# Performance work log

Hardware: AMD Instinct MI355X
Metric: run time of the kernel (lower is better)

Reference implementation:

```python
import jax, jax.numpy as jnp
import numpy as np

B, S, D, H = 8, 2048, 1024, 16
HD = D // H  # head_dim = 64


def setup_inputs() -> dict:
    key = jax.random.key(0)
    ks = jax.random.split(key, 10)
    s = 0.02
    return {
        "x": jax.random.normal(ks[0], (B, S, D), jnp.float32),
        "mask": jnp.zeros((B, 1, S), jnp.float32),
        "Wq": jax.random.normal(ks[1], (D, D), jnp.float32) * s,
        "bq": jnp.zeros((D,), jnp.float32),
        "Wk": jax.random.normal(ks[2], (D, D), jnp.float32) * s,
        "bk": jnp.zeros((D,), jnp.float32),
        "Wv": jax.random.normal(ks[3], (D, D), jnp.float32) * s,
        "bv": jnp.zeros((D,), jnp.float32),
        "wa": jax.random.normal(ks[4], (HD, 1), jnp.float32) * s,
        "ba": jnp.zeros((1,), jnp.float32),
        "wb": jax.random.normal(ks[5], (HD, 1), jnp.float32) * s,
        "bb": jnp.zeros((1,), jnp.float32),
        "Wu": jax.random.normal(ks[6], (HD, HD), jnp.float32) * s,
        "bu": jnp.zeros((HD,), jnp.float32),
        "Wo": jax.random.normal(ks[7], (D, D), jnp.float32) * s,
        "bo": jnp.zeros((D,), jnp.float32),
        "gamma": jnp.ones((D,), jnp.float32),
        "beta_ln": jnp.zeros((D,), jnp.float32),
    }


def _split_heads(t):
    # [B,S,D] -> [B,H,S,HD]
    return t.reshape(B, S, H, HD).transpose(0, 2, 1, 3)


def reference(x, mask, Wq, bq, Wk, bk, Wv, bv, wa, ba, wb, bb, Wu, bu, Wo, bo, gamma, beta_ln):
    scale = 1.0 / jnp.sqrt(jnp.float32(HD))
    q = _split_heads(x @ Wq + bq)  # [B,H,S,HD]
    k = _split_heads(x @ Wk + bk)
    v = _split_heads(x @ Wv + bv)

    # additive attention over queries -> global query vector per head
    alphascore = (jnp.squeeze(q @ wa, -1) + ba[0]) * scale + mask  # [B,H,S]
    alphaw = jax.nn.softmax(alphascore, axis=-1)
    q_av = jnp.einsum('bhs,bhsd->bhd', alphaw, q)

    p = k * q_av[:, :, None, :]  # gated keys [B,H,S,HD]
    betascore = (jnp.squeeze(p @ wb, -1) + bb[0]) * scale + mask
    betaw = jax.nn.softmax(betascore, axis=-1)
    p_av = jnp.einsum('bhs,bhsd->bhd', betaw, p)

    u = v * p_av[:, :, None, :]  # gated values
    r = u @ Wu + bu  # [B,H,S,HD]
    newr = (r + q).transpose(0, 2, 1, 3).reshape(B, S, D)
    attn_out = newr @ Wo + bo

    h = x + attn_out
    mu = jnp.mean(h, axis=-1, keepdims=True)
    var = jnp.mean(jnp.square(h - mu), axis=-1, keepdims=True)
    return (h - mu) * jax.lax.rsqrt(var + 1e-6) * gamma + beta_ln
```

## Files before the change

kernel.cpp:

```cpp
#include <hip/hip_runtime.h>
#include <cstdint>

#define BB 8
#define SS 2048
#define DD 1024
#define HH 16
#define HDIM 64
#define MTOT (BB*SS)
#define NQKV 3072

typedef __attribute__((ext_vector_type(8))) __bf16 bf16x8;
typedef __attribute__((ext_vector_type(4))) float f32x4;

#define AS1(p) ((const __attribute__((address_space(1))) void*)(p))
#define AS3(p) ((__attribute__((address_space(3))) void*)(p))

__device__ __forceinline__ float bf2f(uint16_t u){
  return __uint_as_float(((uint32_t)u) << 16);
}
__device__ __forceinline__ uint16_t f2bf(float f){
  uint32_t u = __float_as_uint(f);
  return (uint16_t)((u + 0x7fffu + ((u >> 16) & 1u)) >> 16);
}

__global__ __launch_bounds__(256)
void k_prep(const float* __restrict__ x,
            const float* __restrict__ Wq, const float* __restrict__ Wk,
            const float* __restrict__ Wv, const float* __restrict__ Wo,
            const float* __restrict__ bq, const float* __restrict__ bk,
            const float* __restrict__ bv,
            uint16_t* __restrict__ xb, uint16_t* __restrict__ Wt,
            uint16_t* __restrict__ WoT, float* __restrict__ bqkv)
{
  __shared__ float t[32][33];
  const int blk = blockIdx.x, tid = threadIdx.x;
  if (blk < 2048){
    const int n4 = MTOT*DD/4;
    for (int i = blk*256 + tid; i < n4; i += 2048*256){
      float4 v = reinterpret_cast<const float4*>(x)[i];
      ushort4 o;
      o.x = f2bf(v.x); o.y = f2bf(v.y); o.z = f2bf(v.z); o.w = f2bf(v.w);
      reinterpret_cast<ushort4*>(xb)[i] = o;
    }
  } else if (blk < 6144){
    const int zb = blk - 2048;
    const int z = zb >> 10, rem = zb & 1023;
    const int by = rem >> 5, bx = rem & 31;
    const float* src = (z==0)?Wq:(z==1)?Wk:(z==2)?Wv:Wo;
    uint16_t* dst = (z<3) ? (Wt + (size_t)z*1024*1024) : WoT;
    const int k0 = by*32, n0 = bx*32;
    const int tx = tid & 31, ty = tid >> 5;
    #pragma unroll
    for (int r = 0; r < 4; ++r)
      t[ty + r*8][tx] = src[(size_t)(k0 + ty + r*8)*1024 + n0 + tx];
    __syncthreads();
    #pragma unroll
    for (int r = 0; r < 4; ++r)
      dst[(size_t)(n0 + ty + r*8)*1024 + k0 + tx] = f2bf(t[tx][ty + r*8]);
  } else {
    const int i = (blk - 6144)*256 + tid;
    if (i < NQKV)
      bqkv[i] = (i < 1024) ? bq[i] : (i < 2048) ? bk[i-1024] : bv[i-2048];
  }
}

#define BARRIER __builtin_amdgcn_s_barrier()

#define READA(BUF, MH) { \
  const uint16_t* _sl = lds + ((BUF)*4 + (MH))*8192; \
  _Pragma("unroll") \
  for (int f = 0; f < 4; ++f) \
    _Pragma("unroll") \
    for (int ks = 0; ks < 2; ++ks) \
      a[f][ks] = *(const bf16x8*)(_sl + (wm*64 + f*16 + l15)*64 + (((ks*4 + l4) ^ l7)<<3)); \
}

#define READB(BUF, NH, BV) { \
  const uint16_t* _sl = lds + ((BUF)*4 + 2 + (NH))*8192; \
  _Pragma("unroll") \
  for (int j = 0; j < 2; ++j) \
    _Pragma("unroll") \
    for (int ks = 0; ks < 2; ++ks) \
      BV[j][ks] = *(const bf16x8*)(_sl + (wn*32 + j*16 + l15)*64 + (((ks*4 + l4) ^ l7)<<3)); \
}

#define MMA(MH, NH, BV) { \
  __builtin_amdgcn_s_setprio(1); \
  _Pragma("unroll") \
  for (int ks = 0; ks < 2; ++ks) \
    _Pragma("unroll") \
    for (int f = 0; f < 4; ++f) \
      _Pragma("unroll") \
      for (int j = 0; j < 2; ++j) \
        acc[(MH)*4+f][(NH)*2+j] = __builtin_amdgcn_mfma_f32_16x16x32_bf16(a[f][ks], BV[j][ks], acc[(MH)*4+f][(NH)*2+j], 0, 0, 0); \
  __builtin_amdgcn_s_setprio(0); }

#define STAGEA(T, H) { \
  char* _d = (char*)lds + ((((T)&1)*4 + (H))*16384) + wave*1024; \
  _Pragma("unroll") \
  for (int l = 0; l < 2; ++l) \
    __builtin_amdgcn_global_load_lds(AS1(pA + (l*131072 + (H)*65536 + (T)*64)), AS3(_d + l*8192), 16, 0, 0); \
}

#define STAGEB(T, H) { \
  char* _d = (char*)lds + ((((T)&1)*4 + 2 + (H))*16384) + wave*1024; \
  _Pragma("unroll") \
  for (int l = 0; l < 2; ++l) \
    __builtin_amdgcn_global_load_lds(AS1(pB + (l*131072 + (H)*32768 + (T)*64)), AS3(_d + l*8192), 16, 0, 0); \
}

template<int EPI, int NB_T>
__global__ __launch_bounds__(512)
void k_gemm256(const uint16_t* __restrict__ A, const uint16_t* __restrict__ Bt,
               const float* __restrict__ bias, const uint16_t* __restrict__ resid16,
               uint16_t* __restrict__ Cout,
               const float* __restrict__ waP, const float* __restrict__ baP,
               const float* __restrict__ maskP,
               float* __restrict__ cpartA, float* __restrict__ dpartA)
{
  constexpr int N = NB_T * 256;
  __shared__ uint16_t lds[8 * 8192];
  const int tid = threadIdx.x;
  const int lane = tid & 63, wave = tid >> 6;
  const int wm = wave >> 2, wn = wave & 3;
  const int l15 = lane & 15, l4 = lane >> 4, l7 = lane & 7;

  const int nwg = gridDim.x, cpx = nwg >> 3, bid = blockIdx.x;
  const int wg = (bid & 7) * cpx + (bid >> 3);
  const int m0 = (wg / NB_T) << 8, n0 = (wg % NB_T) << 8;

  const int colbase = (((tid & 7) ^ ((tid >> 3) & 7)) << 3);
  const uint16_t* pA = A  + (size_t)(m0 + (tid >> 3)) * 1024 + colbase;
  const uint16_t* pB = Bt + (size_t)(n0 + ((tid >> 8) << 6) + ((tid >> 3) & 31)) * 1024 + colbase;

  f32x4 acc[8][4] = {};
  bf16x8 a[4][2], b0[2][2], b1[2][2];

  STAGEA(0,0); STAGEB(0,1); STAGEA(0,1); STAGEB(0,0);
  STAGEA(1,0); STAGEB(1,1); STAGEA(1,1);
  asm volatile("s_waitcnt vmcnt(6)" ::: "memory");
  BARRIER;

  #pragma unroll
  for (int I = 0; I < 7; ++I){
    const int e = 2*I;
    READA(0,0); READB(0,0,b0); STAGEB(e+1, 0);
    BARRIER; MMA(0,0,b0); BARRIER;
    READB(0,1,b1); STAGEA(e+2, 0);
    BARRIER; MMA(0,1,b1); BARRIER;
    READA(0,1); STAGEB(e+2, 1);
    BARRIER; MMA(1,1,b1); BARRIER;
    STAGEA(e+2, 1);
    asm volatile("s_waitcnt vmcnt(6)" ::: "memory");
    BARRIER; MMA(1,0,b0); BARRIER;
    READA(1,0); READB(1,0,b0); STAGEB(e+2, 0);
    BARRIER; MMA(0,0,b0); BARRIER;
    READB(1,1,b1); STAGEA(e+3, 0);
    BARRIER; MMA(0,1,b1); BARRIER;
    READA(1,1); STAGEB(e+3, 1);
    BARRIER; MMA(1,1,b1); BARRIER;
    STAGEA(e+3, 1);
    asm volatile("s_waitcnt vmcnt(6)" ::: "memory");
    BARRIER; MMA(1,0,b0); BARRIER;
  }

  {
    READA(0,0); READB(0,0,b0); STAGEB(15, 0);
    BARRIER; MMA(0,0,b0); BARRIER;
    READB(0,1,b1);
    BARRIER; MMA(0,1,b1); BARRIER;
    READA(0,1);
    BARRIER; MMA(1,1,b1); BARRIER;
    asm volatile("s_waitcnt vmcnt(0)" ::: "memory");
    BARRIER; MMA(1,0,b0); BARRIER;
    READA(1,0); READB(1,0,b0);
    BARRIER; MMA(0,0,b0); BARRIER;
    READB(1,1,b1);
    BARRIER; MMA(0,1,b1); BARRIER;
    READA(1,1);
    BARRIER; MMA(1,1,b1); BARRIER;
    MMA(1,0,b0);
  }

  #pragma unroll
  for (int mh = 0; mh < 2; ++mh)
  #pragma unroll
  for (int f = 0; f < 4; ++f)
  #pragma unroll
  for (int nh = 0; nh < 2; ++nh)
  #pragma unroll
  for (int j = 0; j < 2; ++j){
    const int gcol = n0 + wn*64 + nh*32 + j*16 + l15;
    const float bi = bias[gcol];
    const int rbase = m0 + wm*128 + mh*64 + f*16 + l4*4;
    #pragma unroll
    for (int rr = 0; rr < 4; ++rr){
      const size_t idx = (size_t)(rbase + rr)*N + gcol;
      float v = acc[mh*4+f][nh*2+j][rr] + bi;
      if (EPI == 1) v += bf2f(resid16[idx]);
      Cout[idx] = f2bf(v);
    }
  }

  if (EPI == 0 && n0 < 1024){
    const int hg = (n0 >> 6) + wn;
    const float bav = baP[0];
    float bcol[2][2], wv[2][2];
    #pragma unroll
    for (int nh = 0; nh < 2; ++nh)
    #pragma unroll
    for (int j = 0; j < 2; ++j){
      const int c = nh*32 + j*16 + l15;
      bcol[nh][j] = bias[n0 + wn*64 + c];
      wv[nh][j]   = waP[c];
    }
    float colacc[2][2] = {{0.f,0.f},{0.f,0.f}};
    float esum = 0.f;
    #pragma unroll
    for (int mh = 0; mh < 2; ++mh)
    #pragma unroll
    for (int f = 0; f < 4; ++f)
    #pragma unroll
    for (int rr = 0; rr < 4; ++rr){
      float qv[2][2];
      float p = 0.f;
      #pragma unroll
      for (int nh = 0; nh < 2; ++nh)
      #pragma unroll
      for (int j = 0; j < 2; ++j){
        qv[nh][j] = acc[mh*4+f][nh*2+j][rr] + bcol[nh][j];
        p += qv[nh][j] * wv[nh][j];
      }
      p += __shfl_xor(p, 1); p += __shfl_xor(p, 2);
      p += __shfl_xor(p, 4); p += __shfl_xor(p, 8);
      const int grow = m0 + wm*128 + mh*64 + f*16 + l4*4 + rr;
      const float E = __expf((p + bav)*0.125f + maskP[grow]);
      esum += E;
      #pragma unroll
      for (int nh = 0; nh < 2; ++nh)
      #pragma unroll
      for (int j = 0; j < 2; ++j)
        colacc[nh][j] += E * qv[nh][j];
    }
    const int rb = (m0 >> 7) + wm;
    #pragma unroll
    for (int nh = 0; nh < 2; ++nh)
    #pragma unroll
    for (int j = 0; j < 2; ++j){
      float v = colacc[nh][j];
      v += __shfl_xor(v, 16); v += __shfl_xor(v, 32);
      if (l4 == 0)
        cpartA[(size_t)rb*1024 + n0 + wn*64 + nh*32 + j*16 + l15] = v;
    }
    esum += __shfl_xor(esum, 16); esum += __shfl_xor(esum, 32);
    if (lane == 0) dpartA[rb*16 + hg] = esum;
  }
}

__global__ __launch_bounds__(256)
void k_mergeA(const float* __restrict__ cpartA, const float* __restrict__ dpartA,
              const float* __restrict__ wb,
              float* __restrict__ qavB, float* __restrict__ wvecB)
{
  __shared__ float dsum[16];
  const int blk = blockIdx.x, tid = threadIdx.x;
  const int b = blk >> 2, c = (blk & 3)*256 + tid;
  if (tid < 16){
    float d = 0.f;
    #pragma unroll
    for (int rb = 0; rb < 16; ++rb) d += dpartA[(b*16 + rb)*16 + tid];
    dsum[tid] = d;
  }
  __syncthreads();
  float s = 0.f;
  #pragma unroll
  for (int rb = 0; rb < 16; ++rb) s += cpartA[(size_t)(b*16 + rb)*1024 + c];
  const float qv = s / dsum[(c >> 6) & 15];
  qavB[b*1024 + c]  = qv;
  wvecB[b*1024 + c] = qv * wb[c & 63];
}

__global__ __launch_bounds__(256)
void k_poolB(const uint16_t* __restrict__ qkv, const float* __restrict__ mask,
             const float* __restrict__ bbP, const float* __restrict__ wvecB,
             float* __restrict__ cpartB, float* __restrict__ dpartB)
{
  __shared__ float probe[1024];
  const int blk = blockIdx.x, tid = threadIdx.x;
  const int r0 = blk*32, b = r0 >> 11;
  #pragma unroll
  for (int k2 = 0; k2 < 4; ++k2)
    probe[k2*256 + tid] = wvecB[b*1024 + k2*256 + tid];
  __syncthreads();
  const float bias = bbP[0];
  const uint16_t* base = qkv + 1024;
  const int c0 = tid*4;
  const float p0 = probe[c0], p1 = probe[c0+1], p2 = probe[c0+2], p3 = probe[c0+3];
  float a0 = 0.f, a1 = 0.f, a2 = 0.f, a3 = 0.f, dsum = 0.f;
  for (int r = 0; r < 32; ++r){
    const int row = r0 + r;
    const ushort4 raw = *(const ushort4*)(base + (size_t)row*NQKV + c0);
    const float v0 = bf2f(raw.x), v1 = bf2f(raw.y), v2 = bf2f(raw.z), v3 = bf2f(raw.w);
    float s = v0*p0 + v1*p1 + v2*p2 + v3*p3;
    s += __shfl_xor(s, 1); s += __shfl_xor(s, 2);
    s += __shfl_xor(s, 4); s += __shfl_xor(s, 8);
    const float E = __expf((s + bias)*0.125f + mask[row]);
    a0 += v0*E; a1 += v1*E; a2 += v2*E; a3 += v3*E;
    dsum += E;
  }
  float* cp = cpartB + (size_t)blk*1024 + c0;
  cp[0] = a0; cp[1] = a1; cp[2] = a2; cp[3] = a3;
  if ((tid & 15) == 0) dpartB[blk*16 + (tid >> 4)] = dsum;
}

__global__ __launch_bounds__(256)
void k_mergeB(const float* __restrict__ cpartB, const float* __restrict__ dpartB,
              const float* __restrict__ qavB, const float* __restrict__ Wu,
              uint16_t* __restrict__ WuPT)
{
  __shared__ float red[4][64];
  __shared__ float dsh[4];
  __shared__ float pav[64];
  const int bh = blockIdx.x, b = bh >> 4, h = bh & 15;
  const int tid = threadIdx.x, j = tid & 63, pg = tid >> 6;
  float s = 0.f;
  #pragma unroll
  for (int p = 0; p < 16; ++p)
    s += cpartB[(size_t)(b*64 + pg*16 + p)*1024 + h*64 + j];
  red[pg][j] = s;
  if (j == 0){
    float d = 0.f;
    #pragma unroll
    for (int p = 0; p < 16; ++p) d += dpartB[(b*64 + pg*16 + p)*16 + h];
    dsh[pg] = d;
  }
  __syncthreads();
  if (tid < 64){
    const float cs = red[0][tid] + red[1][tid] + red[2][tid] + red[3][tid];
    const float dd = dsh[0] + dsh[1] + dsh[2] + dsh[3];
    pav[tid] = qavB[b*1024 + h*64 + tid] * (cs / dd);
  }
  __syncthreads();
  uint16_t* dst = WuPT + (size_t)bh*4096;
  for (int idx = tid; idx < 4096; idx += 256){
    const int i = idx & 63, jcol = idx >> 6;
    dst[idx] = f2bf(pav[i]*Wu[i*64 + jcol]);
  }
}

__global__ __launch_bounds__(256)
void k_newr(const uint16_t* __restrict__ qkv, const uint16_t* __restrict__ WuPT,
            const float* __restrict__ bu, uint16_t* __restrict__ newr)
{
  const int bh = blockIdx.x >> 3, st = blockIdx.x & 7;
  const int b = bh >> 4, h = bh & 15;
  const int tid = threadIdx.x, wave = tid >> 6, lane = tid & 63;
  const int l15 = lane & 15, l4 = lane >> 4;
  const int s0 = st*256 + wave*64;
  const uint16_t* vb = qkv + 2048 + h*64;
  const uint16_t* wt = WuPT + (size_t)bh*4096;

  f32x4 acc[4][4] = {};
  #pragma unroll
  for (int ks = 0; ks < 2; ++ks){
    bf16x8 bfr[4];
    #pragma unroll
    for (int n = 0; n < 4; ++n)
      bfr[n] = *(const bf16x8*)(wt + (n*16 + l15)*64 + ks*32 + l4*8);
    #pragma unroll
    for (int m = 0; m < 4; ++m){
      const int s = s0 + m*16 + l15;
      bf16x8 af = *(const bf16x8*)(vb + (size_t)(b*SS + s)*NQKV + ks*32 + l4*8);
      #pragma unroll
      for (int n = 0; n < 4; ++n)
        acc[m][n] = __builtin_amdgcn_mfma_f32_16x16x32_bf16(af, bfr[n], acc[m][n], 0, 0, 0);
    }
  }
  #pragma unroll
  for (int n = 0; n < 4; ++n){
    const int j = n*16 + l15;
    const float bj = bu[j];
    #pragma unroll
    for (int m = 0; m < 4; ++m){
      #pragma unroll
      for (int r = 0; r < 4; ++r){
        const int s = s0 + m*16 + l4*4 + r;
        const size_t qidx = (size_t)(b*SS + s)*NQKV + h*64 + j;
        const float q = bf2f(qkv[qidx]);
        newr[(size_t)(b*SS + s)*DD + h*64 + j] = f2bf(acc[m][n][r] + bj + q);
      }
    }
  }
}

__global__ __launch_bounds__(256)
void k_ln(const uint16_t* __restrict__ h16, const float* __restrict__ gamma,
          const float* __restrict__ beta, float* __restrict__ out)
{
  __shared__ float r1[256], r2[256];
  const int row = blockIdx.x, tid = threadIdx.x;
  const ushort4 hv = ((const ushort4*)(h16 + (size_t)row*DD))[tid];
  float v0 = bf2f(hv.x), v1 = bf2f(hv.y), v2 = bf2f(hv.z), v3 = bf2f(hv.w);
  float s  = v0 + v1 + v2 + v3;
  float ss = v0*v0 + v1*v1 + v2*v2 + v3*v3;
  r1[tid] = s; r2[tid] = ss; __syncthreads();
  for (int off = 128; off > 0; off >>= 1){
    if (tid < off){ r1[tid] += r1[tid+off]; r2[tid] += r2[tid+off]; }
    __syncthreads();
  }
  const float mu  = r1[0]*(1.f/1024.f);
  const float var = r2[0]*(1.f/1024.f) - mu*mu;
  const float inv = rsqrtf(var + 1e-6f);
  const float4 g  = ((const float4*)gamma)[tid];
  const float4 be = ((const float4*)beta)[tid];
  float4 o;
  o.x = (v0-mu)*inv*g.x + be.x;
  o.y = (v1-mu)*inv*g.y + be.y;
  o.z = (v2-mu)*inv*g.z + be.z;
  o.w = (v3-mu)*inv*g.w + be.w;
  ((float4*)(out + (size_t)row*DD))[tid] = o;
}

extern "C" void kernel_launch(void* const* d_in, const int* in_sizes, int n_in,
                              void* d_out, int out_size, void* d_ws, size_t ws_size,
                              hipStream_t stream) {
  const float* x    = (const float*)d_in[0];
  const float* mask = (const float*)d_in[1];
  const float* Wq   = (const float*)d_in[2];
  const float* bq   = (const float*)d_in[3];
  const float* Wk   = (const float*)d_in[4];
  const float* bk   = (const float*)d_in[5];
  const float* Wv   = (const float*)d_in[6];
  const float* bv   = (const float*)d_in[7];
  const float* wa   = (const float*)d_in[8];
  const float* ba   = (const float*)d_in[9];
  const float* wb   = (const float*)d_in[10];
  const float* bb   = (const float*)d_in[11];
  const float* Wu   = (const float*)d_in[12];
  const float* bu   = (const float*)d_in[13];
  const float* Wo   = (const float*)d_in[14];
  const float* bo   = (const float*)d_in[15];
  const float* gamma= (const float*)d_in[16];
  const float* beta = (const float*)d_in[17];
  float* out = (float*)d_out;

  char* ws = (char*)d_ws;
  const size_t MB = 1ull << 20;
  uint16_t* xb    = (uint16_t*)(ws);
  uint16_t* Wt    = (uint16_t*)(ws + 32*MB);
  uint16_t* WoT   = (uint16_t*)(ws + 38*MB);
  float*    bqkv  = (float*)   (ws + 40*MB);
  uint16_t* WuPT  = (uint16_t*)(ws + 41*MB);
  uint16_t* qkv   = (uint16_t*)(ws + 42*MB);
  uint16_t* newr  = (uint16_t*)(ws + 138*MB);
  uint16_t* hbuf16= (uint16_t*)(ws + 42*MB);
  float* cpartA = (float*)(ws + 138*MB);
  float* dpartA = (float*)(ws + 139*MB);
  float* cpartB = (float*)(ws + 140*MB);
  float* dpartB = (float*)(ws + 142*MB);
  float* qavB   = (float*)(ws + 143*MB);
  float* wvecB  = (float*)(ws + 144*MB);

  k_prep<<<6156, 256, 0, stream>>>(x, Wq, Wk, Wv, Wo, bq, bk, bv, xb, Wt, WoT, bqkv);

  k_gemm256<0,12><<<(MTOT/256)*(NQKV/256), 512, 0, stream>>>(
      xb, Wt, bqkv, nullptr, qkv, wa, ba, mask, cpartA, dpartA);

  k_mergeA<<<32, 256, 0, stream>>>(cpartA, dpartA, wb, qavB, wvecB);
  k_poolB<<<512, 256, 0, stream>>>(qkv, mask, bb, wvecB, cpartB, dpartB);
  k_mergeB<<<128, 256, 0, stream>>>(cpartB, dpartB, qavB, Wu, WuPT);

  k_newr<<<BB*HH*8, 256, 0, stream>>>(qkv, WuPT, bu, newr);
  k_gemm256<1,4><<<(MTOT/256)*(DD/256), 512, 0, stream>>>(
      newr, WoT, bo, xb, hbuf16, nullptr, nullptr, nullptr, nullptr, nullptr);
  k_ln<<<MTOT, 256, 0, stream>>>(hbuf16, gamma, beta, out);
}
```

Before: 219.4 us.

## Eliminate K projection by folding Wk into beta-pooling via linearity

Drops the K columns from the fused QKV GEMM, shrinking it from 3072 to 2048 output columns. The beta pooling is rewritten algebraically: the score weights are folded through Wk to give per-head probes over x, scores are computed directly from x, and the weighted sum of x is projected through Wk only once per batch and head. This removes a third of the large GEMM and its K writeback. In exchange it adds several small kernels that read x repeatedly, and it changes rounding because K is no longer rounded to bf16 before pooling.

```diff
diff --git a/kernel.cpp b/kernel.cpp
--- a/kernel.cpp
+++ b/kernel.cpp
@@ -7,7 +7,7 @@
 #define HH 16
 #define HDIM 64
 #define MTOT (BB*SS)
-#define NQKV 3072
+#define QKVW 2048
 
 typedef __attribute__((ext_vector_type(8))) __bf16 bf16x8;
 typedef __attribute__((ext_vector_type(4))) float f32x4;
@@ -27,10 +27,10 @@
 void k_prep(const float* __restrict__ x,
             const float* __restrict__ Wq, const float* __restrict__ Wk,
             const float* __restrict__ Wv, const float* __restrict__ Wo,
-            const float* __restrict__ bq, const float* __restrict__ bk,
-            const float* __restrict__ bv,
+            const float* __restrict__ bq, const float* __restrict__ bv,
             uint16_t* __restrict__ xb, uint16_t* __restrict__ Wt,
-            uint16_t* __restrict__ WoT, float* __restrict__ bqkv)
+            uint16_t* __restrict__ Wkt, uint16_t* __restrict__ WoT,
+            float* __restrict__ bqv)
 {
   __shared__ float t[32][33];
   const int blk = blockIdx.x, tid = threadIdx.x;
@@ -46,8 +46,8 @@
     const int zb = blk - 2048;
     const int z = zb >> 10, rem = zb & 1023;
     const int by = rem >> 5, bx = rem & 31;
-    const float* src = (z==0)?Wq:(z==1)?Wk:(z==2)?Wv:Wo;
-    uint16_t* dst = (z<3) ? (Wt + (size_t)z*1024*1024) : WoT;
+    const float* src = (z==0)?Wq:(z==1)?Wv:(z==2)?Wk:Wo;
+    uint16_t* dst = (z==0)?Wt:(z==1)?(Wt + 1024*1024):(z==2)?Wkt:WoT;
     const int k0 = by*32, n0 = bx*32;
     const int tx = tid & 31, ty = tid >> 5;
     #pragma unroll
@@ -59,8 +59,8 @@
       dst[(size_t)(n0 + ty + r*8)*1024 + k0 + tx] = f2bf(t[tx][ty + r*8]);
   } else {
     const int i = (blk - 6144)*256 + tid;
-    if (i < NQKV)
-      bqkv[i] = (i < 1024) ? bq[i] : (i < 2048) ? bk[i-1024] : bv[i-2048];
+    if (i < QKVW)
+      bqv[i] = (i < 1024) ? bq[i] : bv[i-1024];
   }
 }
 
@@ -281,70 +281,164 @@
 }
 
 __global__ __launch_bounds__(256)
-void k_poolB(const uint16_t* __restrict__ qkv, const float* __restrict__ mask,
-             const float* __restrict__ bbP, const float* __restrict__ wvecB,
-             float* __restrict__ cpartB, float* __restrict__ dpartB)
-{
-  __shared__ float probe[1024];
+void k_foldB(const uint16_t* __restrict__ Wkt, const float* __restrict__ wvecB,
+             const float* __restrict__ bk, const float* __restrict__ bbP,
+             float* __restrict__ pBg, float* __restrict__ csB)
+{
+  __shared__ float wl[64];
+  __shared__ float redc[64];
+  const int bh = blockIdx.x, b = bh >> 4, h = bh & 15;
+  const int tid = threadIdx.x;
+  if (tid < 64) wl[tid] = wvecB[b*1024 + h*64 + tid];
+  __syncthreads();
+  const int k0 = tid*4;
+  float a0 = 0.f, a1 = 0.f, a2 = 0.f, a3 = 0.f;
+  for (int d = 0; d < 64; ++d){
+    const float w = wl[d];
+    const ushort4 r = *(const ushort4*)(Wkt + (size_t)(h*64 + d)*1024 + k0);
+    a0 += bf2f(r.x)*w; a1 += bf2f(r.y)*w; a2 += bf2f(r.z)*w; a3 += bf2f(r.w)*w;
+  }
+  float* dst = pBg + (size_t)bh*1024 + k0;
+  dst[0] = a0; dst[1] = a1; dst[2] = a2; dst[3] = a3;
+  if (tid < 64) redc[tid] = bk[h*64 + tid] * wl[tid];
+  __syncthreads();
+  if (tid == 0){
+    float s = 0.f;
+    for (int i = 0; i < 64; ++i) s += redc[i];
+    csB[bh] = s + bbP[0];
+  }
+}
+
+__global__ __launch_bounds__(256)
+void k_scoreB(const uint16_t* __restrict__ xb, const float* __restrict__ pBg,
+              const float* __restrict__ csB, const float* __restrict__ mask,
+              float* __restrict__ EB, float* __restrict__ dpartB)
+{
+  __shared__ float csl[16];
+  __shared__ float sred[32][4][16];
+  __shared__ float EBl[32][16];
   const int blk = blockIdx.x, tid = threadIdx.x;
   const int r0 = blk*32, b = r0 >> 11;
-  #pragma unroll
-  for (int k2 = 0; k2 < 4; ++k2)
-    probe[k2*256 + tid] = wvecB[b*1024 + k2*256 + tid];
-  __syncthreads();
-  const float bias = bbP[0];
-  const uint16_t* base = qkv + 1024;
-  const int c0 = tid*4;
-  const float p0 = probe[c0], p1 = probe[c0+1], p2 = probe[c0+2], p3 = probe[c0+3];
-  float a0 = 0.f, a1 = 0.f, a2 = 0.f, a3 = 0.f, dsum = 0.f;
+  if (tid < 16) csl[tid] = csB[b*16 + tid];
+  const int g = tid >> 4, h = tid & 15, w = tid >> 6;
+  float4 pb[16];
+  #pragma unroll
+  for (int i = 0; i < 16; ++i)
+    pb[i] = *(const float4*)(pBg + (size_t)(b*16 + h)*1024 + g*64 + i*4);
+  __syncthreads();
+  const uint16_t* xr0 = xb + (size_t)r0*1024 + g*64;
   for (int r = 0; r < 32; ++r){
-    const int row = r0 + r;
-    const ushort4 raw = *(const ushort4*)(base + (size_t)row*NQKV + c0);
-    const float v0 = bf2f(raw.x), v1 = bf2f(raw.y), v2 = bf2f(raw.z), v3 = bf2f(raw.w);
-    float s = v0*p0 + v1*p1 + v2*p2 + v3*p3;
-    s += __shfl_xor(s, 1); s += __shfl_xor(s, 2);
-    s += __shfl_xor(s, 4); s += __shfl_xor(s, 8);
-    const float E = __expf((s + bias)*0.125f + mask[row]);
-    a0 += v0*E; a1 += v1*E; a2 += v2*E; a3 += v3*E;
-    dsum += E;
-  }
-  float* cp = cpartB + (size_t)blk*1024 + c0;
-  cp[0] = a0; cp[1] = a1; cp[2] = a2; cp[3] = a3;
-  if ((tid & 15) == 0) dpartB[blk*16 + (tid >> 4)] = dsum;
-}
-
-__global__ __launch_bounds__(256)
-void k_mergeB(const float* __restrict__ cpartB, const float* __restrict__ dpartB,
-              const float* __restrict__ qavB, const float* __restrict__ Wu,
+    const uint16_t* xr = xr0 + (size_t)r*1024;
+    float part = 0.f;
+    #pragma unroll
+    for (int i = 0; i < 8; ++i){
+      bf16x8 v = *(const bf16x8*)(xr + i*8);
+      part += (float)v[0]*pb[2*i].x   + (float)v[1]*pb[2*i].y
+            + (float)v[2]*pb[2*i].z   + (float)v[3]*pb[2*i].w
+            + (float)v[4]*pb[2*i+1].x + (float)v[5]*pb[2*i+1].y
+            + (float)v[6]*pb[2*i+1].z + (float)v[7]*pb[2*i+1].w;
+    }
+    part += __shfl_xor(part, 16); part += __shfl_xor(part, 32);
+    if ((tid & 48) == 0) sred[r][w][h] = part;
+  }
+  __syncthreads();
+  #pragma unroll
+  for (int rr = 0; rr < 2; ++rr){
+    const int idx = rr*256 + tid, r = idx >> 4, hh = idx & 15;
+    const float s = sred[r][0][hh] + sred[r][1][hh] + sred[r][2][hh] + sred[r][3][hh];
+    const float E = __expf((s + csl[hh])*0.125f + mask[r0 + r]);
+    EB[(size_t)(r0 + r)*16 + hh] = E;
+    EBl[r][hh] = E;
+  }
+  __syncthreads();
+  if (tid < 16){
+    float d = 0.f;
+    #pragma unroll
+    for (int r = 0; r < 32; ++r) d += EBl[r][tid];
+    dpartB[blk*16 + tid] = d;
+  }
+}
+
+__global__ __launch_bounds__(256)
+void k_xsumB(const uint16_t* __restrict__ xb, const float* __restrict__ EB,
+             float* __restrict__ xwBp)
+{
+  __shared__ float part[4][16][64];
+  const int blk = blockIdx.x, tid = threadIdx.x;
+  const int b = blk >> 5, ch = (blk >> 1) & 15, rh = blk & 1;
+  const int col = ch*64 + (tid & 63), rg = tid >> 6;
+  float acc[16];
+  #pragma unroll
+  for (int i = 0; i < 16; ++i) acc[i] = 0.f;
+  const int rowbase = b*2048 + rh*1024 + rg*256;
+  for (int r = 0; r < 256; ++r){
+    const int row = rowbase + r;
+    const float xv = bf2f(xb[(size_t)row*1024 + col]);
+    const float4* e4 = (const float4*)(EB + (size_t)row*16);
+    const float4 e0 = e4[0], e1 = e4[1], e2 = e4[2], e3 = e4[3];
+    acc[0] += xv*e0.x; acc[1] += xv*e0.y; acc[2]  += xv*e0.z; acc[3]  += xv*e0.w;
+    acc[4] += xv*e1.x; acc[5] += xv*e1.y; acc[6]  += xv*e1.z; acc[7]  += xv*e1.w;
+    acc[8] += xv*e2.x; acc[9] += xv*e2.y; acc[10] += xv*e2.z; acc[11] += xv*e2.w;
+    acc[12]+= xv*e3.x; acc[13]+= xv*e3.y; acc[14] += xv*e3.z; acc[15] += xv*e3.w;
+  }
+  #pragma unroll
+  for (int hh = 0; hh < 16; ++hh) part[rg][hh][tid & 63] = acc[hh];
+  __syncthreads();
+  #pragma unroll
+  for (int it = 0; it < 4; ++it){
+    const int idx = it*256 + tid, hh = idx >> 6, c = idx & 63;
+    const float s = part[0][hh][c] + part[1][hh][c] + part[2][hh][c] + part[3][hh][c];
+    xwBp[((size_t)(b*2 + rh)*16 + hh)*1024 + ch*64 + c] = s;
+  }
+}
+
+__global__ __launch_bounds__(256)
+void k_finalB(const float* __restrict__ xwBp, const float* __restrict__ dpartB,
+              const float* __restrict__ qavB, const uint16_t* __restrict__ Wkt,
+              const float* __restrict__ bk, const float* __restrict__ Wu,
               uint16_t* __restrict__ WuPT)
 {
-  __shared__ float red[4][64];
-  __shared__ float dsh[4];
-  __shared__ float pav[64];
+  __shared__ float xwl[1024];
+  __shared__ float kvl[64];
+  __shared__ float pavl[64];
+  __shared__ float dsh;
   const int bh = blockIdx.x, b = bh >> 4, h = bh & 15;
-  const int tid = threadIdx.x, j = tid & 63, pg = tid >> 6;
+  const int tid = threadIdx.x;
+  #pragma unroll
+  for (int i = 0; i < 4; ++i){
+    const int idx = i*256 + tid;
+    xwl[idx] = xwBp[((size_t)(b*2 + 0)*16 + h)*1024 + idx]
+             + xwBp[((size_t)(b*2 + 1)*16 + h)*1024 + idx];
+  }
+  if (tid < 64){
+    float d = dpartB[(b*64 + tid)*16 + h];
+    d += __shfl_xor(d, 1);  d += __shfl_xor(d, 2);  d += __shfl_xor(d, 4);
+    d += __shfl_xor(d, 8);  d += __shfl_xor(d, 16); d += __shfl_xor(d, 32);
+    if (tid == 0) dsh = d;
+  }
+  __syncthreads();
+  const int d = tid >> 2, q = tid & 3;
+  const uint16_t* wrow = Wkt + (size_t)(h*64 + d)*1024 + q*256;
+  const float* xwq = xwl + q*256;
   float s = 0.f;
   #pragma unroll
-  for (int p = 0; p < 16; ++p)
-    s += cpartB[(size_t)(b*64 + pg*16 + p)*1024 + h*64 + j];
-  red[pg][j] = s;
-  if (j == 0){
-    float d = 0.f;
-    #pragma unroll
-    for (int p = 0; p < 16; ++p) d += dpartB[(b*64 + pg*16 + p)*16 + h];
-    dsh[pg] = d;
-  }
-  __syncthreads();
-  if (tid < 64){
-    const float cs = red[0][tid] + red[1][tid] + red[2][tid] + red[3][tid];
-    const float dd = dsh[0] + dsh[1] + dsh[2] + dsh[3];
-    pav[tid] = qavB[b*1024 + h*64 + tid] * (cs / dd);
-  }
+  for (int i = 0; i < 32; ++i){
+    bf16x8 v = *(const bf16x8*)(wrow + i*8);
+    s += (float)v[0]*xwq[i*8+0] + (float)v[1]*xwq[i*8+1]
+       + (float)v[2]*xwq[i*8+2] + (float)v[3]*xwq[i*8+3]
+       + (float)v[4]*xwq[i*8+4] + (float)v[5]*xwq[i*8+5]
+       + (float)v[6]*xwq[i*8+6] + (float)v[7]*xwq[i*8+7];
+  }
+  s += __shfl_xor(s, 1); s += __shfl_xor(s, 2);
+  if (q == 0) kvl[d] = s;
+  __syncthreads();
+  if (tid < 64)
+    pavl[tid] = qavB[b*1024 + h*64 + tid] * (kvl[tid]/dsh + bk[h*64 + tid]);
   __syncthreads();
   uint16_t* dst = WuPT + (size_t)bh*4096;
   for (int idx = tid; idx < 4096; idx += 256){
     const int i = idx & 63, jcol = idx >> 6;
-    dst[idx] = f2bf(pav[i]*Wu[i*64 + jcol]);
+    dst[idx] = f2bf(pavl[i]*Wu[i*64 + jcol]);
   }
 }
 
@@ -357,7 +451,7 @@
   const int tid = threadIdx.x, wave = tid >> 6, lane = tid & 63;
   const int l15 = lane & 15, l4 = lane >> 4;
   const int s0 = st*256 + wave*64;
-  const uint16_t* vb = qkv + 2048 + h*64;
+  const uint16_t* vb = qkv + 1024 + h*64;
   const uint16_t* wt = WuPT + (size_t)bh*4096;
 
   f32x4 acc[4][4] = {};
@@ -370,7 +464,7 @@
     #pragma unroll
     for (int m = 0; m < 4; ++m){
       const int s = s0 + m*16 + l15;
-      bf16x8 af = *(const bf16x8*)(vb + (size_t)(b*SS + s)*NQKV + ks*32 + l4*8);
+      bf16x8 af = *(const bf16x8*)(vb + (size_t)(b*SS + s)*QKVW + ks*32 + l4*8);
       #pragma unroll
       for (int n = 0; n < 4; ++n)
         acc[m][n] = __builtin_amdgcn_mfma_f32_16x16x32_bf16(af, bfr[n], acc[m][n], 0, 0, 0);
@@ -385,7 +479,7 @@
       #pragma unroll
       for (int r = 0; r < 4; ++r){
         const int s = s0 + m*16 + l4*4 + r;
-        const size_t qidx = (size_t)(b*SS + s)*NQKV + h*64 + j;
+        const size_t qidx = (size_t)(b*SS + s)*QKVW + h*64 + j;
         const float q = bf2f(qkv[qidx]);
         newr[(size_t)(b*SS + s)*DD + h*64 + j] = f2bf(acc[m][n][r] + bj + q);
       }
@@ -448,27 +542,33 @@
   const size_t MB = 1ull << 20;
   uint16_t* xb    = (uint16_t*)(ws);
   uint16_t* Wt    = (uint16_t*)(ws + 32*MB);
+  uint16_t* Wkt   = (uint16_t*)(ws + 36*MB);
   uint16_t* WoT   = (uint16_t*)(ws + 38*MB);
-  float*    bqkv  = (float*)   (ws + 40*MB);
+  float*    bqv   = (float*)   (ws + 40*MB);
   uint16_t* WuPT  = (uint16_t*)(ws + 41*MB);
   uint16_t* qkv   = (uint16_t*)(ws + 42*MB);
-  uint16_t* newr  = (uint16_t*)(ws + 138*MB);
   uint16_t* hbuf16= (uint16_t*)(ws + 42*MB);
-  float* cpartA = (float*)(ws + 138*MB);
-  float* dpartA = (float*)(ws + 139*MB);
-  float* cpartB = (float*)(ws + 140*MB);
-  float* dpartB = (float*)(ws + 142*MB);
-  float* qavB   = (float*)(ws + 143*MB);
-  float* wvecB  = (float*)(ws + 144*MB);
-
-  k_prep<<<6156, 256, 0, stream>>>(x, Wq, Wk, Wv, Wo, bq, bk, bv, xb, Wt, WoT, bqkv);
-
-  k_gemm256<0,12><<<(MTOT/256)*(NQKV/256), 512, 0, stream>>>(
-      xb, Wt, bqkv, nullptr, qkv, wa, ba, mask, cpartA, dpartA);
+  float* cpartA = (float*)(ws + 110*MB);
+  float* dpartA = (float*)(ws + 111*MB);
+  float* qavB   = (float*)(ws + 112*MB);
+  float* wvecB  = (float*)(ws + 113*MB);
+  float* pBg    = (float*)(ws + 114*MB);
+  float* csB    = (float*)(ws + 115*MB);
+  float* EB     = (float*)(ws + 116*MB);
+  float* dpartB = (float*)(ws + 118*MB);
+  float* xwBp   = (float*)(ws + 119*MB);
+  uint16_t* newr= (uint16_t*)(ws + 138*MB);
+
+  k_prep<<<6156, 256, 0, stream>>>(x, Wq, Wk, Wv, Wo, bq, bv, xb, Wt, Wkt, WoT, bqv);
+
+  k_gemm256<0,8><<<(MTOT/256)*(QKVW/256), 512, 0, stream>>>(
+      xb, Wt, bqv, nullptr, qkv, wa, ba, mask, cpartA, dpartA);
 
   k_mergeA<<<32, 256, 0, stream>>>(cpartA, dpartA, wb, qavB, wvecB);
-  k_poolB<<<512, 256, 0, stream>>>(qkv, mask, bb, wvecB, cpartB, dpartB);
-  k_mergeB<<<128, 256, 0, stream>>>(cpartB, dpartB, qavB, Wu, WuPT);
+  k_foldB<<<128, 256, 0, stream>>>(Wkt, wvecB, bk, bb, pBg, csB);
+  k_scoreB<<<512, 256, 0, stream>>>(xb, pBg, csB, mask, EB, dpartB);
+  k_xsumB<<<256, 256, 0, stream>>>(xb, EB, xwBp);
+  k_finalB<<<128, 256, 0, stream>>>(xwBp, dpartB, qavB, Wkt, bk, Wu, WuPT);
 
   k_newr<<<BB*HH*8, 256, 0, stream>>>(qkv, WuPT, bu, newr);
   k_gemm256<1,4><<<(MTOT/256)*(DD/256), 512, 0, stream>>>(
```

Measured after the change: 278.5 us. 26.9% more time.
